# Optimization experiments

Hardware: AMD Instinct MI355X
Metric: run time of the kernel (lower is better)

The kernel has to match this reference:

```python
import jax, jax.numpy as jnp
import numpy as np

OUTPUT_LEN = 180  # decoder steps, from __init__ default


def gru_cell(x, h, Wih, Whh, bih, bhh):
    """PyTorch-convention GRU cell. x:(B,in) h:(B,H) -> (B,H)."""
    gi = x @ Wih.T + bih          # (B,3H)
    gh = h @ Whh.T + bhh          # (B,3H)
    ir, iz, inn = jnp.split(gi, 3, axis=-1)
    hr, hz, hn = jnp.split(gh, 3, axis=-1)
    r = jax.nn.sigmoid(ir + hr)
    z = jax.nn.sigmoid(iz + hz)
    n = jnp.tanh(inn + r * hn)
    return (1.0 - z) * n + z * h


def setup_inputs() -> dict:
    key = jax.random.key(0)
    B, T_in, N_IN, H = 8192, 512, 2, 64
    ks = jax.random.split(key, 20)
    s = 0.05
    d = {
        "x": jax.random.normal(ks[0], (B, T_in, N_IN), jnp.float32),
        "enc_Wih0": jax.random.normal(ks[1], (3 * H, N_IN), jnp.float32) * s,
        "enc_Whh0": jax.random.normal(ks[2], (3 * H, H), jnp.float32) * s,
        "enc_bih0": jax.random.normal(ks[3], (3 * H,), jnp.float32) * s,
        "enc_bhh0": jax.random.normal(ks[4], (3 * H,), jnp.float32) * s,
        "enc_Wih1": jax.random.normal(ks[5], (3 * H, H), jnp.float32) * s,
        "enc_Whh1": jax.random.normal(ks[6], (3 * H, H), jnp.float32) * s,
        "enc_bih1": jax.random.normal(ks[7], (3 * H,), jnp.float32) * s,
        "enc_bhh1": jax.random.normal(ks[8], (3 * H,), jnp.float32) * s,
        "dec_Wih0": jax.random.normal(ks[9], (3 * H, 1), jnp.float32) * s,
        "dec_Whh0": jax.random.normal(ks[10], (3 * H, H), jnp.float32) * s,
        "dec_bih0": jax.random.normal(ks[11], (3 * H,), jnp.float32) * s,
        "dec_bhh0": jax.random.normal(ks[12], (3 * H,), jnp.float32) * s,
        "dec_Wih1": jax.random.normal(ks[13], (3 * H, H), jnp.float32) * s,
        "dec_Whh1": jax.random.normal(ks[14], (3 * H, H), jnp.float32) * s,
        "dec_bih1": jax.random.normal(ks[15], (3 * H,), jnp.float32) * s,
        "dec_bhh1": jax.random.normal(ks[16], (3 * H,), jnp.float32) * s,
        "out_W": jax.random.normal(ks[17], (1, H), jnp.float32) * s,
        "out_b": jax.random.normal(ks[18], (1,), jnp.float32) * s,
    }
    return d


def reference(x, enc_Wih0, enc_Whh0, enc_bih0, enc_bhh0,
              enc_Wih1, enc_Whh1, enc_bih1, enc_bhh1,
              dec_Wih0, dec_Whh0, dec_bih0, dec_bhh0,
              dec_Wih1, dec_Whh1, dec_bih1, dec_bhh1,
              out_W, out_b):
    B = x.shape[0]
    H = enc_Whh0.shape[1]
    h0 = jnp.zeros((B, H), x.dtype)
    h1 = jnp.zeros((B, H), x.dtype)

    # ---- encoder: 2-layer GRU over input_len steps ----
    def enc_step(carry, xt):
        h0, h1 = carry
        h0 = gru_cell(xt, h0, enc_Wih0, enc_Whh0, enc_bih0, enc_bhh0)
        h1 = gru_cell(h0, h1, enc_Wih1, enc_Whh1, enc_bih1, enc_bhh1)
        return (h0, h1), None

    (h0, h1), _ = jax.lax.scan(enc_step, (h0, h1), jnp.swapaxes(x, 0, 1))

    prev = jnp.zeros((B, 1), x.dtype)

    def dec_step(carry, _):
        h0, h1, prev = carry
        h0 = gru_cell(prev, h0, dec_Wih0, dec_Whh0, dec_bih0, dec_bhh0)
        h1 = gru_cell(h0, h1, dec_Wih1, dec_Whh1, dec_bih1, dec_bhh1)
        cv = h1 @ out_W.T + out_b          # (B,1)
        return (h0, h1, cv), cv

    _, ys = jax.lax.scan(dec_step, (h0, h1, prev), None, length=OUTPUT_LEN)
    # ys: (T, B, 1) -> (B, T, 1)
    return jnp.swapaxes(ys, 0, 1)
```

## Files before the change

kernel.cpp:

```cpp
#include <hip/hip_runtime.h>


typedef __attribute__((ext_vector_type(8))) short bf16x8;
typedef __attribute__((ext_vector_type(4))) float f32x4;

struct Params {
  const float *x;
  const float *wih0e, *bih0e, *bhh0e, *bih1e, *bhh1e;
  const float *wih0d, *bih0d, *bhh0d, *bih1d, *bhh1d;
  const float *outW, *outb;
  const unsigned short *wt;
  float *out;
};

__device__ __forceinline__ float sgm(float v) { return 1.f / (1.f + __expf(-v)); }
__device__ __forceinline__ float th(float v)  { float e = __expf(2.f * v); return 1.f - 2.f / (e + 1.f); }

__device__ __forceinline__ unsigned short rbf(float v) {
  unsigned int u = __float_as_uint(v);
  return (unsigned short)((u + 0x7fffu + ((u >> 16) & 1u)) >> 16);
}
__device__ __forceinline__ float ubf(unsigned short h) {
  return __uint_as_float((unsigned int)h << 16);
}

__device__ __forceinline__ f32x4 mfma16(bf16x8 a, bf16x8 b, f32x4 c) {
  return __builtin_amdgcn_mfma_f32_16x16x32_bf16(a, b, c, 0, 0, 0);
}

__global__ void prep_w(const float* s0, const float* s1, const float* s2,
                       const float* s3, const float* s4, const float* s5,
                       unsigned short* dst) {
  const float* srcs[6] = {s0, s1, s2, s3, s4, s5};
  const float* s = srcs[blockIdx.x];
  unsigned short* o = dst + blockIdx.x * 24576;
  for (int i = threadIdx.x; i < 24576; i += blockDim.x) {
    int e  = i & 7;
    int l  = (i >> 3) & 63;
    int sp = (i >> 9) & 1;
    int kf = (i >> 10) & 1;
    int nt = i >> 11;
    int n = nt * 16 + (l & 15);
    int k = kf * 32 + (l >> 4) * 8 + e;
    float v = s[n * 64 + k];
    unsigned short hi = rbf(v);
    unsigned short val = hi;
    if (sp) val = rbf(v - ubf(hi));
    o[i] = val;
  }
}


__global__ __launch_bounds__(256) __attribute__((amdgpu_waves_per_eu(2, 2)))
void gru_main(Params p) {
  __shared__ unsigned short aH0[2][2048];
  __shared__ unsigned short aH1[2][2048];
  __shared__ float pw[4][16];

  const int tid = threadIdx.x;
  const int l   = tid & 63;
  const int w   = tid >> 6;
  const int jc  = l & 15;
  const int rg  = l >> 4;
  const int j   = w * 16 + jc;
  const int b0  = blockIdx.x * 16;

  const int kfj = j >> 5, rgj = (j >> 3) & 3, ej = j & 7;
  const int wbase = kfj * 1024 + rgj * 128 + ej;
  const int rdb = rg * 128 + ((jc ^ rg) << 3);

  for (int i = tid; i < 2048; i += 256) {
    aH0[0][i] = 0; aH0[1][i] = 0; aH1[0][i] = 0; aH1[1][i] = 0;
  }
  float h0own[4] = {0.f, 0.f, 0.f, 0.f}, h1own[4] = {0.f, 0.f, 0.f, 0.f};

  bf16x8 wB[3][3][2][2];

  for (int ph = 0; ph < 2; ++ph) {
#pragma unroll
    for (int m = 0; m < 3; ++m)
#pragma unroll
      for (int g = 0; g < 3; ++g)
#pragma unroll
        for (int kf = 0; kf < 2; ++kf)
#pragma unroll
          for (int sp = 0; sp < 2; ++sp) {
            int nt = g * 4 + w;
            wB[m][g][kf][sp] = *(const bf16x8*)(p.wt +
                (((((ph * 3 + m) * 12 + nt) * 2 + kf) * 2 + sp) << 9) + l * 8);
          }
    float bi0[3], bh0[3], bi1[3], bh1[3], wxa[3], wxb[3];
#pragma unroll
    for (int g = 0; g < 3; ++g) {
      int r = g * 64 + j;
      if (ph == 0) {
        bi0[g] = p.bih0e[r]; bh0[g] = p.bhh0e[r];
        bi1[g] = p.bih1e[r]; bh1[g] = p.bhh1e[r];
        wxa[g] = p.wih0e[2 * r]; wxb[g] = p.wih0e[2 * r + 1];
      } else {
        bi0[g] = p.bih0d[r]; bh0[g] = p.bhh0d[r];
        bi1[g] = p.bih1d[r]; bh1[g] = p.bhh1d[r];
        wxa[g] = p.wih0d[r]; wxb[g] = 0.f;
      }
    }
    const float oW = p.outW[j], ob = p.outb[0];
    const int T = ph ? 180 : 512;
    __syncthreads();

    for (int t = 0; t < T; ++t) {
      const int cur = t & 1;
      float2 xx[4]; float prevv[4];
      if (ph == 0) {
#pragma unroll
        for (int i = 0; i < 4; ++i)
          xx[i] = *(const float2*)(p.x + ((size_t)(b0 + rg * 4 + i) * 512 + t) * 2);
      } else {
        if (t > 0) {
#pragma unroll
          for (int i = 0; i < 4; ++i)
            prevv[i] = ob + pw[0][rg * 4 + i] + pw[1][rg * 4 + i]
                          + pw[2][rg * 4 + i] + pw[3][rg * 4 + i];
          if (w == 0 && jc == 0) {
#pragma unroll
            for (int i = 0; i < 4; ++i)
              p.out[(size_t)(b0 + rg * 4 + i) * 180 + (t - 1)] = prevv[i];
          }
        } else {
#pragma unroll
          for (int i = 0; i < 4; ++i) prevv[i] = 0.f;
        }
      }
      const unsigned short* h0o = aH0[cur ^ 1];
      f32x4 aR = {0,0,0,0}, aZ = {0,0,0,0}, aN = {0,0,0,0};
#pragma unroll
      for (int kf = 0; kf < 2; ++kf) {
        bf16x8 ah = *(const bf16x8*)&h0o[kf * 1024 + rdb];
        bf16x8 al = *(const bf16x8*)&h0o[kf * 1024 + 512 + rdb];
        aR = mfma16(ah, wB[0][0][kf][0], aR);
        aZ = mfma16(ah, wB[0][1][kf][0], aZ);
        aN = mfma16(ah, wB[0][2][kf][0], aN);
        aR = mfma16(al, wB[0][0][kf][0], aR);
        aZ = mfma16(al, wB[0][1][kf][0], aZ);
        aN = mfma16(al, wB[0][2][kf][0], aN);
        aR = mfma16(ah, wB[0][0][kf][1], aR);
        aZ = mfma16(ah, wB[0][1][kf][1], aZ);
        aN = mfma16(ah, wB[0][2][kf][1], aN);
      }
      unsigned short* h0n = aH0[cur];
#pragma unroll
      for (int i = 0; i < 4; ++i) {
        float xr, xz, xn;
        if (ph == 0) {
          xr = bi0[0] + wxa[0] * xx[i].x + wxb[0] * xx[i].y;
          xz = bi0[1] + wxa[1] * xx[i].x + wxb[1] * xx[i].y;
          xn = bi0[2] + wxa[2] * xx[i].x + wxb[2] * xx[i].y;
        } else {
          xr = bi0[0] + wxa[0] * prevv[i];
          xz = bi0[1] + wxa[1] * prevv[i];
          xn = bi0[2] + wxa[2] * prevv[i];
        }
        float r = sgm(xr + bh0[0] + aR[i]);
        float z = sgm(xz + bh0[1] + aZ[i]);
        float n = th(xn + r * (bh0[2] + aN[i]));
        h0own[i] = (1.f - z) * n + z * h0own[i];
        unsigned short hi = rbf(h0own[i]);
        unsigned short lo = rbf(h0own[i] - ubf(hi));
        int idx = wbase + (((rg * 4 + i) ^ rgj) << 3);
        h0n[idx] = hi; h0n[idx + 512] = lo;
      }
      __syncthreads();
      const unsigned short* h1o = aH1[cur ^ 1];
      f32x4 iR = {0,0,0,0}, iZ = {0,0,0,0}, iN = {0,0,0,0};
      f32x4 hR = {0,0,0,0}, hZ = {0,0,0,0}, hN = {0,0,0,0};
#pragma unroll
      for (int kf = 0; kf < 2; ++kf) {
        bf16x8 gh = *(const bf16x8*)&h0n[kf * 1024 + rdb];
        bf16x8 gl = *(const bf16x8*)&h0n[kf * 1024 + 512 + rdb];
        bf16x8 qh = *(const bf16x8*)&h1o[kf * 1024 + rdb];
        bf16x8 ql = *(const bf16x8*)&h1o[kf * 1024 + 512 + rdb];
        iR = mfma16(gh, wB[1][0][kf][0], iR);
        hR = mfma16(qh, wB[2][0][kf][0], hR);
        iZ = mfma16(gh, wB[1][1][kf][0], iZ);
        hZ = mfma16(qh, wB[2][1][kf][0], hZ);
        iN = mfma16(gh, wB[1][2][kf][0], iN);
        hN = mfma16(qh, wB[2][2][kf][0], hN);
        iR = mfma16(gl, wB[1][0][kf][0], iR);
        hR = mfma16(ql, wB[2][0][kf][0], hR);
        iZ = mfma16(gl, wB[1][1][kf][0], iZ);
        hZ = mfma16(ql, wB[2][1][kf][0], hZ);
        iN = mfma16(gl, wB[1][2][kf][0], iN);
        hN = mfma16(ql, wB[2][2][kf][0], hN);
        iR = mfma16(gh, wB[1][0][kf][1], iR);
        hR = mfma16(qh, wB[2][0][kf][1], hR);
        iZ = mfma16(gh, wB[1][1][kf][1], iZ);
        hZ = mfma16(qh, wB[2][1][kf][1], hZ);
        iN = mfma16(gh, wB[1][2][kf][1], iN);
        hN = mfma16(qh, wB[2][2][kf][1], hN);
      }
      unsigned short* h1n = aH1[cur];
      float v[4];
#pragma unroll
      for (int i = 0; i < 4; ++i) {
        float r = sgm(iR[i] + hR[i] + bi1[0] + bh1[0]);
        float z = sgm(iZ[i] + hZ[i] + bi1[1] + bh1[1]);
        float n = th(iN[i] + bi1[2] + r * (bh1[2] + hN[i]));
        h1own[i] = (1.f - z) * n + z * h1own[i];
        unsigned short hi = rbf(h1own[i]);
        unsigned short lo = rbf(h1own[i] - ubf(hi));
        int idx = wbase + (((rg * 4 + i) ^ rgj) << 3);
        h1n[idx] = hi; h1n[idx + 512] = lo;
        v[i] = oW * h1own[i];
      }
      if (ph == 1) {
#pragma unroll
        for (int off = 1; off < 16; off <<= 1)
#pragma unroll
          for (int i = 0; i < 4; ++i) v[i] += __shfl_xor(v[i], off, 64);
        if (jc == 0) {
#pragma unroll
          for (int i = 0; i < 4; ++i) pw[w][rg * 4 + i] = v[i];
        }
      }
      __syncthreads();
    }
    if (ph == 1) {
      if (w == 0 && jc == 0) {
#pragma unroll
        for (int i = 0; i < 4; ++i) {
          float fv = ob + pw[0][rg * 4 + i] + pw[1][rg * 4 + i]
                        + pw[2][rg * 4 + i] + pw[3][rg * 4 + i];
          p.out[(size_t)(b0 + rg * 4 + i) * 180 + 179] = fv;
        }
      }
    }
  }
}

extern "C" void kernel_launch(void* const* d_in, const int* in_sizes, int n_in,
                              void* d_out, int out_size, void* d_ws, size_t ws_size,
                              hipStream_t stream) {
  unsigned short* wt = (unsigned short*)d_ws;

  prep_w<<<dim3(6), dim3(256), 0, stream>>>(
      (const float*)d_in[2], (const float*)d_in[5], (const float*)d_in[6],
      (const float*)d_in[10], (const float*)d_in[13], (const float*)d_in[14], wt);

  Params p;
  p.x = (const float*)d_in[0];
  p.wih0e = (const float*)d_in[1];
  p.bih0e = (const float*)d_in[3];
  p.bhh0e = (const float*)d_in[4];
  p.bih1e = (const float*)d_in[7];
  p.bhh1e = (const float*)d_in[8];
  p.wih0d = (const float*)d_in[9];
  p.bih0d = (const float*)d_in[11];
  p.bhh0d = (const float*)d_in[12];
  p.bih1d = (const float*)d_in[15];
  p.bhh1d = (const float*)d_in[16];
  p.outW = (const float*)d_in[17];
  p.outb = (const float*)d_in[18];
  p.wt = wt;
  p.out = (float*)d_out;

  gru_main<<<dim3(512), dim3(256), 0, stream>>>(p);
}
```

Baseline: 2.154 ms.

## Split GRU K-dimension across wave pairs with LDS partial-sum exchange

Each block now handles 32 batch rows with 512 threads. Eight waves split the hidden-size contraction in half (kf), so each wave keeps only half the weight fragments, pinned in AGPRs via asm constraints. Each wave computes partial MFMA products for both 16-row batch halves, then exchanges the partials through a shared buffer so every wave finishes gates for its own rows. The aim is to cut per-wave register pressure and shorten the serial MFMA chain per step, at the cost of an extra barrier and extra LDS traffic in each layer of each timestep.

```diff
diff --git a/kernel.cpp b/kernel.cpp
--- a/kernel.cpp
+++ b/kernel.cpp
@@ -51,56 +51,58 @@
 }
 
 
-__global__ __launch_bounds__(256) __attribute__((amdgpu_waves_per_eu(2, 2)))
-void gru_main(Params p) {
-  __shared__ unsigned short aH0[2][2048];
-  __shared__ unsigned short aH1[2][2048];
-  __shared__ float pw[4][16];
+__global__ __launch_bounds__(512, 2) void gru_main(Params p) {
+  __shared__ unsigned short aH0[2][2][2048];
+  __shared__ unsigned short aH1[2][2][2048];
+  __shared__ f32x4 ex[8][7][64];
+  __shared__ float pw[4][32];
 
   const int tid = threadIdx.x;
   const int l   = tid & 63;
   const int w   = tid >> 6;
+  const int g   = w & 3;
+  const int kf  = w >> 2;
   const int jc  = l & 15;
   const int rg  = l >> 4;
-  const int j   = w * 16 + jc;
-  const int b0  = blockIdx.x * 16;
+  const int j   = g * 16 + jc;
+  const int b0  = blockIdx.x * 32;
+  const int bloc = kf * 16 + rg * 4;
 
   const int kfj = j >> 5, rgj = (j >> 3) & 3, ej = j & 7;
-  const int wbase = kfj * 1024 + rgj * 128 + ej;
-  const int rdb = rg * 128 + ((jc ^ rg) << 3);
-
-  for (int i = tid; i < 2048; i += 256) {
-    aH0[0][i] = 0; aH0[1][i] = 0; aH1[0][i] = 0; aH1[1][i] = 0;
+  const int wbase = kf * 2048 + kfj * 1024 + rgj * 128 + ej;
+  const int rdb = kf * 1024 + rg * 128 + ((jc ^ rg) << 3);
+
+  for (int i = tid; i < 8192; i += 512) {
+    ((unsigned short*)aH0)[i] = 0;
+    ((unsigned short*)aH1)[i] = 0;
   }
   float h0own[4] = {0.f, 0.f, 0.f, 0.f}, h1own[4] = {0.f, 0.f, 0.f, 0.f};
 
-  bf16x8 wB[3][3][2][2];
+  bf16x8 wB[3][3][2];
 
   for (int ph = 0; ph < 2; ++ph) {
 #pragma unroll
     for (int m = 0; m < 3; ++m)
 #pragma unroll
-      for (int g = 0; g < 3; ++g)
-#pragma unroll
-        for (int kf = 0; kf < 2; ++kf)
-#pragma unroll
-          for (int sp = 0; sp < 2; ++sp) {
-            int nt = g * 4 + w;
-            wB[m][g][kf][sp] = *(const bf16x8*)(p.wt +
-                (((((ph * 3 + m) * 12 + nt) * 2 + kf) * 2 + sp) << 9) + l * 8);
-          }
+      for (int gt = 0; gt < 3; ++gt)
+#pragma unroll
+        for (int sp = 0; sp < 2; ++sp) {
+          int nt = gt * 4 + g;
+          wB[m][gt][sp] = *(const bf16x8*)(p.wt +
+              (((((ph * 3 + m) * 12 + nt) * 2 + kf) * 2 + sp) << 9) + l * 8);
+        }
     float bi0[3], bh0[3], bi1[3], bh1[3], wxa[3], wxb[3];
 #pragma unroll
-    for (int g = 0; g < 3; ++g) {
-      int r = g * 64 + j;
+    for (int gt = 0; gt < 3; ++gt) {
+      int r = gt * 64 + j;
       if (ph == 0) {
-        bi0[g] = p.bih0e[r]; bh0[g] = p.bhh0e[r];
-        bi1[g] = p.bih1e[r]; bh1[g] = p.bhh1e[r];
-        wxa[g] = p.wih0e[2 * r]; wxb[g] = p.wih0e[2 * r + 1];
+        bi0[gt] = p.bih0e[r]; bh0[gt] = p.bhh0e[r];
+        bi1[gt] = p.bih1e[r]; bh1[gt] = p.bhh1e[r];
+        wxa[gt] = p.wih0e[2 * r]; wxb[gt] = p.wih0e[2 * r + 1];
       } else {
-        bi0[g] = p.bih0d[r]; bh0[g] = p.bhh0d[r];
-        bi1[g] = p.bih1d[r]; bh1[g] = p.bhh1d[r];
-        wxa[g] = p.wih0d[r]; wxb[g] = 0.f;
+        bi0[gt] = p.bih0d[r]; bh0[gt] = p.bhh0d[r];
+        bi1[gt] = p.bih1d[r]; bh1[gt] = p.bhh1d[r];
+        wxa[gt] = p.wih0d[r]; wxb[gt] = 0.f;
       }
     }
     const float oW = p.outW[j], ob = p.outb[0];
@@ -108,128 +110,197 @@
     __syncthreads();
 
     for (int t = 0; t < T; ++t) {
+#pragma unroll
+      for (int m = 0; m < 3; ++m)
+#pragma unroll
+        for (int gt = 0; gt < 3; ++gt)
+#pragma unroll
+          for (int sp = 0; sp < 2; ++sp)
+            asm volatile("" : "+a"(wB[m][gt][sp]));
+
       const int cur = t & 1;
+      const unsigned short* h0o = &aH0[cur ^ 1][0][0];
+      const unsigned short* h1o = &aH1[cur ^ 1][0][0];
+      unsigned short* h0n = &aH0[cur][0][0];
+      unsigned short* h1n = &aH1[cur][0][0];
+
+      f32x4 aR0 = {0,0,0,0}, aZ0 = {0,0,0,0}, aN0 = {0,0,0,0};
+      f32x4 aR1 = {0,0,0,0}, aZ1 = {0,0,0,0}, aN1 = {0,0,0,0};
+      {
+        bf16x8 ah0 = *(const bf16x8*)&h0o[rdb];
+        bf16x8 al0 = *(const bf16x8*)&h0o[rdb + 512];
+        bf16x8 ah1 = *(const bf16x8*)&h0o[2048 + rdb];
+        bf16x8 al1 = *(const bf16x8*)&h0o[2048 + rdb + 512];
+        aR0 = mfma16(ah0, wB[0][0][0], aR0);
+        aR1 = mfma16(ah1, wB[0][0][0], aR1);
+        aZ0 = mfma16(ah0, wB[0][1][0], aZ0);
+        aZ1 = mfma16(ah1, wB[0][1][0], aZ1);
+        aN0 = mfma16(ah0, wB[0][2][0], aN0);
+        aN1 = mfma16(ah1, wB[0][2][0], aN1);
+        aR0 = mfma16(al0, wB[0][0][0], aR0);
+        aR1 = mfma16(al1, wB[0][0][0], aR1);
+        aZ0 = mfma16(al0, wB[0][1][0], aZ0);
+        aZ1 = mfma16(al1, wB[0][1][0], aZ1);
+        aN0 = mfma16(al0, wB[0][2][0], aN0);
+        aN1 = mfma16(al1, wB[0][2][0], aN1);
+        aR0 = mfma16(ah0, wB[0][0][1], aR0);
+        aR1 = mfma16(ah1, wB[0][0][1], aR1);
+        aZ0 = mfma16(ah0, wB[0][1][1], aZ0);
+        aZ1 = mfma16(ah1, wB[0][1][1], aZ1);
+        aN0 = mfma16(ah0, wB[0][2][1], aN0);
+        aN1 = mfma16(ah1, wB[0][2][1], aN1);
+      }
+      ex[w][0][l] = kf ? aR0 : aR1;
+      ex[w][1][l] = kf ? aZ0 : aZ1;
+      ex[w][2][l] = kf ? aN0 : aN1;
+      __syncthreads();
+
       float2 xx[4]; float prevv[4];
       if (ph == 0) {
 #pragma unroll
         for (int i = 0; i < 4; ++i)
-          xx[i] = *(const float2*)(p.x + ((size_t)(b0 + rg * 4 + i) * 512 + t) * 2);
+          xx[i] = *(const float2*)(p.x + ((size_t)(b0 + bloc + i) * 512 + t) * 2);
+      } else if (t > 0) {
+#pragma unroll
+        for (int i = 0; i < 4; ++i)
+          prevv[i] = ob + pw[0][bloc + i] + pw[1][bloc + i]
+                        + pw[2][bloc + i] + pw[3][bloc + i];
+        if (g == 0 && jc == 0) {
+#pragma unroll
+          for (int i = 0; i < 4; ++i)
+            p.out[(size_t)(b0 + bloc + i) * 180 + (t - 1)] = prevv[i];
+        }
       } else {
-        if (t > 0) {
-#pragma unroll
-          for (int i = 0; i < 4; ++i)
-            prevv[i] = ob + pw[0][rg * 4 + i] + pw[1][rg * 4 + i]
-                          + pw[2][rg * 4 + i] + pw[3][rg * 4 + i];
-          if (w == 0 && jc == 0) {
-#pragma unroll
-            for (int i = 0; i < 4; ++i)
-              p.out[(size_t)(b0 + rg * 4 + i) * 180 + (t - 1)] = prevv[i];
+#pragma unroll
+        for (int i = 0; i < 4; ++i) prevv[i] = 0.f;
+      }
+      {
+        f32x4 sR = kf ? aR1 : aR0;
+        f32x4 sZ = kf ? aZ1 : aZ0;
+        f32x4 sN = kf ? aN1 : aN0;
+        f32x4 pR = ex[w ^ 4][0][l];
+        f32x4 pZ = ex[w ^ 4][1][l];
+        f32x4 pN = ex[w ^ 4][2][l];
+#pragma unroll
+        for (int i = 0; i < 4; ++i) {
+          float xr, xz, xn;
+          if (ph == 0) {
+            xr = bi0[0] + wxa[0] * xx[i].x + wxb[0] * xx[i].y;
+            xz = bi0[1] + wxa[1] * xx[i].x + wxb[1] * xx[i].y;
+            xn = bi0[2] + wxa[2] * xx[i].x + wxb[2] * xx[i].y;
+          } else {
+            xr = bi0[0] + wxa[0] * prevv[i];
+            xz = bi0[1] + wxa[1] * prevv[i];
+            xn = bi0[2] + wxa[2] * prevv[i];
           }
-        } else {
-#pragma unroll
-          for (int i = 0; i < 4; ++i) prevv[i] = 0.f;
-        }
-      }
-      const unsigned short* h0o = aH0[cur ^ 1];
-      f32x4 aR = {0,0,0,0}, aZ = {0,0,0,0}, aN = {0,0,0,0};
-#pragma unroll
-      for (int kf = 0; kf < 2; ++kf) {
-        bf16x8 ah = *(const bf16x8*)&h0o[kf * 1024 + rdb];
-        bf16x8 al = *(const bf16x8*)&h0o[kf * 1024 + 512 + rdb];
-        aR = mfma16(ah, wB[0][0][kf][0], aR);
-        aZ = mfma16(ah, wB[0][1][kf][0], aZ);
-        aN = mfma16(ah, wB[0][2][kf][0], aN);
-        aR = mfma16(al, wB[0][0][kf][0], aR);
-        aZ = mfma16(al, wB[0][1][kf][0], aZ);
-        aN = mfma16(al, wB[0][2][kf][0], aN);
-        aR = mfma16(ah, wB[0][0][kf][1], aR);
-        aZ = mfma16(ah, wB[0][1][kf][1], aZ);
-        aN = mfma16(ah, wB[0][2][kf][1], aN);
-      }
-      unsigned short* h0n = aH0[cur];
-#pragma unroll
-      for (int i = 0; i < 4; ++i) {
-        float xr, xz, xn;
-        if (ph == 0) {
-          xr = bi0[0] + wxa[0] * xx[i].x + wxb[0] * xx[i].y;
-          xz = bi0[1] + wxa[1] * xx[i].x + wxb[1] * xx[i].y;
-          xn = bi0[2] + wxa[2] * xx[i].x + wxb[2] * xx[i].y;
-        } else {
-          xr = bi0[0] + wxa[0] * prevv[i];
-          xz = bi0[1] + wxa[1] * prevv[i];
-          xn = bi0[2] + wxa[2] * prevv[i];
-        }
-        float r = sgm(xr + bh0[0] + aR[i]);
-        float z = sgm(xz + bh0[1] + aZ[i]);
-        float n = th(xn + r * (bh0[2] + aN[i]));
-        h0own[i] = (1.f - z) * n + z * h0own[i];
-        unsigned short hi = rbf(h0own[i]);
-        unsigned short lo = rbf(h0own[i] - ubf(hi));
-        int idx = wbase + (((rg * 4 + i) ^ rgj) << 3);
-        h0n[idx] = hi; h0n[idx + 512] = lo;
+          float r = sgm(xr + bh0[0] + sR[i] + pR[i]);
+          float z = sgm(xz + bh0[1] + sZ[i] + pZ[i]);
+          float n = th(xn + r * (bh0[2] + sN[i] + pN[i]));
+          h0own[i] = (1.f - z) * n + z * h0own[i];
+          unsigned short hi = rbf(h0own[i]);
+          unsigned short lo = rbf(h0own[i] - ubf(hi));
+          int idx = wbase + (((rg * 4 + i) ^ rgj) << 3);
+          h0n[idx] = hi; h0n[idx + 512] = lo;
+        }
       }
       __syncthreads();
-      const unsigned short* h1o = aH1[cur ^ 1];
-      f32x4 iR = {0,0,0,0}, iZ = {0,0,0,0}, iN = {0,0,0,0};
-      f32x4 hR = {0,0,0,0}, hZ = {0,0,0,0}, hN = {0,0,0,0};
-#pragma unroll
-      for (int kf = 0; kf < 2; ++kf) {
-        bf16x8 gh = *(const bf16x8*)&h0n[kf * 1024 + rdb];
-        bf16x8 gl = *(const bf16x8*)&h0n[kf * 1024 + 512 + rdb];
-        bf16x8 qh = *(const bf16x8*)&h1o[kf * 1024 + rdb];
-        bf16x8 ql = *(const bf16x8*)&h1o[kf * 1024 + 512 + rdb];
-        iR = mfma16(gh, wB[1][0][kf][0], iR);
-        hR = mfma16(qh, wB[2][0][kf][0], hR);
-        iZ = mfma16(gh, wB[1][1][kf][0], iZ);
-        hZ = mfma16(qh, wB[2][1][kf][0], hZ);
-        iN = mfma16(gh, wB[1][2][kf][0], iN);
-        hN = mfma16(qh, wB[2][2][kf][0], hN);
-        iR = mfma16(gl, wB[1][0][kf][0], iR);
-        hR = mfma16(ql, wB[2][0][kf][0], hR);
-        iZ = mfma16(gl, wB[1][1][kf][0], iZ);
-        hZ = mfma16(ql, wB[2][1][kf][0], hZ);
-        iN = mfma16(gl, wB[1][2][kf][0], iN);
-        hN = mfma16(ql, wB[2][2][kf][0], hN);
-        iR = mfma16(gh, wB[1][0][kf][1], iR);
-        hR = mfma16(qh, wB[2][0][kf][1], hR);
-        iZ = mfma16(gh, wB[1][1][kf][1], iZ);
-        hZ = mfma16(qh, wB[2][1][kf][1], hZ);
-        iN = mfma16(gh, wB[1][2][kf][1], iN);
-        hN = mfma16(qh, wB[2][2][kf][1], hN);
-      }
-      unsigned short* h1n = aH1[cur];
-      float v[4];
-#pragma unroll
-      for (int i = 0; i < 4; ++i) {
-        float r = sgm(iR[i] + hR[i] + bi1[0] + bh1[0]);
-        float z = sgm(iZ[i] + hZ[i] + bi1[1] + bh1[1]);
-        float n = th(iN[i] + bi1[2] + r * (bh1[2] + hN[i]));
-        h1own[i] = (1.f - z) * n + z * h1own[i];
-        unsigned short hi = rbf(h1own[i]);
-        unsigned short lo = rbf(h1own[i] - ubf(hi));
-        int idx = wbase + (((rg * 4 + i) ^ rgj) << 3);
-        h1n[idx] = hi; h1n[idx + 512] = lo;
-        v[i] = oW * h1own[i];
-      }
-      if (ph == 1) {
-#pragma unroll
-        for (int off = 1; off < 16; off <<= 1)
-#pragma unroll
-          for (int i = 0; i < 4; ++i) v[i] += __shfl_xor(v[i], off, 64);
-        if (jc == 0) {
-#pragma unroll
-          for (int i = 0; i < 4; ++i) pw[w][rg * 4 + i] = v[i];
+
+      f32x4 cR0 = {0,0,0,0}, cZ0 = {0,0,0,0}, iN0 = {0,0,0,0}, hN0 = {0,0,0,0};
+      f32x4 cR1 = {0,0,0,0}, cZ1 = {0,0,0,0}, iN1 = {0,0,0,0}, hN1 = {0,0,0,0};
+      {
+        bf16x8 gh0 = *(const bf16x8*)&h0n[rdb];
+        bf16x8 gl0 = *(const bf16x8*)&h0n[rdb + 512];
+        bf16x8 gh1 = *(const bf16x8*)&h0n[2048 + rdb];
+        bf16x8 gl1 = *(const bf16x8*)&h0n[2048 + rdb + 512];
+        bf16x8 qh0 = *(const bf16x8*)&h1o[rdb];
+        bf16x8 ql0 = *(const bf16x8*)&h1o[rdb + 512];
+        bf16x8 qh1 = *(const bf16x8*)&h1o[2048 + rdb];
+        bf16x8 ql1 = *(const bf16x8*)&h1o[2048 + rdb + 512];
+        cR0 = mfma16(gh0, wB[1][0][0], cR0);
+        cR1 = mfma16(gh1, wB[1][0][0], cR1);
+        cZ0 = mfma16(gh0, wB[1][1][0], cZ0);
+        cZ1 = mfma16(gh1, wB[1][1][0], cZ1);
+        iN0 = mfma16(gh0, wB[1][2][0], iN0);
+        iN1 = mfma16(gh1, wB[1][2][0], iN1);
+        cR0 = mfma16(qh0, wB[2][0][0], cR0);
+        cR1 = mfma16(qh1, wB[2][0][0], cR1);
+        cZ0 = mfma16(qh0, wB[2][1][0], cZ0);
+        cZ1 = mfma16(qh1, wB[2][1][0], cZ1);
+        hN0 = mfma16(qh0, wB[2][2][0], hN0);
+        hN1 = mfma16(qh1, wB[2][2][0], hN1);
+        cR0 = mfma16(gl0, wB[1][0][0], cR0);
+        cR1 = mfma16(gl1, wB[1][0][0], cR1);
+        cZ0 = mfma16(gl0, wB[1][1][0], cZ0);
+        cZ1 = mfma16(gl1, wB[1][1][0], cZ1);
+        iN0 = mfma16(gl0, wB[1][2][0], iN0);
+        iN1 = mfma16(gl1, wB[1][2][0], iN1);
+        cR0 = mfma16(ql0, wB[2][0][0], cR0);
+        cR1 = mfma16(ql1, wB[2][0][0], cR1);
+        cZ0 = mfma16(ql0, wB[2][1][0], cZ0);
+        cZ1 = mfma16(ql1, wB[2][1][0], cZ1);
+        hN0 = mfma16(ql0, wB[2][2][0], hN0);
+        hN1 = mfma16(ql1, wB[2][2][0], hN1);
+        cR0 = mfma16(gh0, wB[1][0][1], cR0);
+        cR1 = mfma16(gh1, wB[1][0][1], cR1);
+        cZ0 = mfma16(gh0, wB[1][1][1], cZ0);
+        cZ1 = mfma16(gh1, wB[1][1][1], cZ1);
+        iN0 = mfma16(gh0, wB[1][2][1], iN0);
+        iN1 = mfma16(gh1, wB[1][2][1], iN1);
+        cR0 = mfma16(qh0, wB[2][0][1], cR0);
+        cR1 = mfma16(qh1, wB[2][0][1], cR1);
+        cZ0 = mfma16(qh0, wB[2][1][1], cZ0);
+        cZ1 = mfma16(qh1, wB[2][1][1], cZ1);
+        hN0 = mfma16(qh0, wB[2][2][1], hN0);
+        hN1 = mfma16(qh1, wB[2][2][1], hN1);
+      }
+      ex[w][3][l] = kf ? cR0 : cR1;
+      ex[w][4][l] = kf ? cZ0 : cZ1;
+      ex[w][5][l] = kf ? iN0 : iN1;
+      ex[w][6][l] = kf ? hN0 : hN1;
+      __syncthreads();
+
+      {
+        f32x4 sR = kf ? cR1 : cR0;
+        f32x4 sZ = kf ? cZ1 : cZ0;
+        f32x4 sI = kf ? iN1 : iN0;
+        f32x4 sH = kf ? hN1 : hN0;
+        f32x4 pR = ex[w ^ 4][3][l];
+        f32x4 pZ = ex[w ^ 4][4][l];
+        f32x4 pI = ex[w ^ 4][5][l];
+        f32x4 pH = ex[w ^ 4][6][l];
+        float v[4];
+#pragma unroll
+        for (int i = 0; i < 4; ++i) {
+          float r = sgm(sR[i] + pR[i] + bi1[0] + bh1[0]);
+          float z = sgm(sZ[i] + pZ[i] + bi1[1] + bh1[1]);
+          float n = th(sI[i] + pI[i] + bi1[2] + r * (bh1[2] + sH[i] + pH[i]));
+          h1own[i] = (1.f - z) * n + z * h1own[i];
+          unsigned short hi = rbf(h1own[i]);
+          unsigned short lo = rbf(h1own[i] - ubf(hi));
+          int idx = wbase + (((rg * 4 + i) ^ rgj) << 3);
+          h1n[idx] = hi; h1n[idx + 512] = lo;
+          v[i] = oW * h1own[i];
+        }
+        if (ph == 1) {
+#pragma unroll
+          for (int off = 1; off < 16; off <<= 1)
+#pragma unroll
+            for (int i = 0; i < 4; ++i) v[i] += __shfl_xor(v[i], off, 64);
+          if (jc == 0) {
+#pragma unroll
+            for (int i = 0; i < 4; ++i) pw[g][bloc + i] = v[i];
+          }
         }
       }
       __syncthreads();
     }
     if (ph == 1) {
-      if (w == 0 && jc == 0) {
+      if (g == 0 && jc == 0) {
 #pragma unroll
         for (int i = 0; i < 4; ++i) {
-          float fv = ob + pw[0][rg * 4 + i] + pw[1][rg * 4 + i]
-                        + pw[2][rg * 4 + i] + pw[3][rg * 4 + i];
-          p.out[(size_t)(b0 + rg * 4 + i) * 180 + 179] = fv;
+          float fv = ob + pw[0][bloc + i] + pw[1][bloc + i]
+                        + pw[2][bloc + i] + pw[3][bloc + i];
+          p.out[(size_t)(b0 + bloc + i) * 180 + 179] = fv;
         }
       }
     }
@@ -262,5 +333,5 @@
   p.wt = wt;
   p.out = (float*)d_out;
 
-  gru_main<<<dim3(512), dim3(256), 0, stream>>>(p);
-}
+  gru_main<<<dim3(256), dim3(512), 0, stream>>>(p);
+}
```

Result: slower. 2.668 ms (+23.9%).
